# Optimization experiments

Hardware: AMD Instinct MI355X
Metric: run time of the kernel (lower is better)

## Reference

```python
import jax, jax.numpy as jnp
import numpy as np

D_MODEL = 1024
NUM_HEADS = 16
WINDOW = 2048  # must equal seq_len (see notes): source matmul attn(B,H,S,W) @ v(B,H,S,hd) requires W == S
SEQ_LEN = 2048
BATCH = 1


def setup_inputs() -> dict:
    key = jax.random.key(0)
    k0, k1, k2 = jax.random.split(key, 3)
    d = D_MODEL
    x = jax.random.normal(k0, (BATCH, SEQ_LEN, d), dtype=jnp.float32)
    w_qkv = jax.random.normal(k1, (3 * d, d), dtype=jnp.float32) * (d ** -0.5)
    b_qkv = jnp.zeros((3 * d,), dtype=jnp.float32)
    w_proj = jax.random.normal(k2, (d, d), dtype=jnp.float32) * (d ** -0.5)
    b_proj = jnp.zeros((d,), dtype=jnp.float32)
    return {"x": x, "w_qkv": w_qkv, "b_qkv": b_qkv, "w_proj": w_proj, "b_proj": b_proj}


def reference(x, w_qkv, b_qkv, w_proj, b_proj):
    B, S, d = x.shape
    H = NUM_HEADS
    hd = d // H
    W = WINDOW
    scale = hd ** -0.5

    # qkv projection (torch Linear: x @ W^T + b)
    qkv = x @ w_qkv.T + b_qkv                      # (B, S, 3d)
    qkv = qkv.reshape(B, S, 3, H, hd).transpose(2, 0, 3, 1, 4)  # (3, B, H, S, hd)
    q, k, v = qkv[0], qkv[1], qkv[2]

    # sliding-window scores: score[b,h,i,j] = q_i . k_padded[i+j] * scale, j in [0, W)
    pad = W // 2
    k_pad = jnp.pad(k, ((0, 0), (0, 0), (pad, pad), (0, 0)))     # (B, H, S+W, hd)
    scores_full = jnp.einsum('bhid,bhjd->bhij', q, k_pad) * scale  # (B, H, S, S+W)
    idx = jnp.arange(S)[:, None] + jnp.arange(W)[None, :]          # (S, W) banded gather indices
    scores = jnp.take_along_axis(scores_full, idx[None, None], axis=-1)  # (B, H, S, W)

    attn = jax.nn.softmax(scores, axis=-1)
    attn = jnp.nan_to_num(attn)  # faithful to torch.nan_to_num(attn, 0.0)

    # Faithful to the source: forward() does matmul(attn, v), i.e. column j of the
    # windowed attn indexes v position j directly (requires W == S).
    out = jnp.einsum('bhij,bhjd->bhid', attn, v)   # (B, H, S, hd)
    out = out.transpose(0, 2, 1, 3).reshape(B, S, d)
    out = out @ w_proj.T + b_proj
    return out, attn
```

## Files before the change

### kernel.cpp

```cpp
#include <hip/hip_runtime.h>
#include <hip/hip_bf16.h>

typedef __hip_bfloat16 bf16;
typedef __attribute__((ext_vector_type(8))) short short8;
typedef __attribute__((ext_vector_type(4))) float f32x4;
typedef __attribute__((ext_vector_type(4))) unsigned short ushort4v;

#define DEV static __device__ __forceinline__

static constexpr int SEQ = 2048;
static constexpr int DM  = 1024;
static constexpr int NH  = 16;
static constexpr int HD  = 64;
static constexpr int WIN = 2048;
static constexpr int PAD = 1024;

DEV void async16(const void* g, void* l) {
  __builtin_amdgcn_global_load_lds(
      (__attribute__((address_space(1))) void*)(g),
      (__attribute__((address_space(3))) void*)(l), 16, 0, 0);
}

__global__ __launch_bounds__(256) void k_cvt(const float* __restrict__ x,
                                             const float* __restrict__ wq,
                                             const float* __restrict__ wp,
                                             bf16* __restrict__ xb,
                                             bf16* __restrict__ wqb,
                                             bf16* __restrict__ wpb) {
  const int NX = SEQ * DM, NQ = 3 * DM * DM, NP = DM * DM;
  const int tot = (NX + NQ + NP) >> 2;
  const int stride = gridDim.x * 256;
  for (int i = blockIdx.x * 256 + threadIdx.x; i < tot; i += stride) {
    int e = i << 2;
    const float* s; bf16* d; int o;
    if (e < NX)            { s = x;  d = xb;  o = e; }
    else if (e < NX + NQ)  { s = wq; d = wqb; o = e - NX; }
    else                   { s = wp; d = wpb; o = e - NX - NQ; }
    float4 v = *(const float4*)(s + o);
    __align__(8) bf16 t4[4] = {__float2bfloat16(v.x), __float2bfloat16(v.y),
                               __float2bfloat16(v.z), __float2bfloat16(v.w)};
    *(uint2*)(d + o) = *(uint2*)t4;
  }
}

DEV void gemm_core64(const bf16* __restrict__ A, const bf16* __restrict__ B,
                     int m0, int n0, int K, int tid, bf16* As, bf16* Bs,
                     f32x4 (&acc)[4][2]) {
  const int lane = tid & 63, wid = tid >> 6;
  const int l15 = lane & 15, l4 = lane >> 4;
  for (int k0 = 0; k0 < K; k0 += 64) {
    __syncthreads();
    #pragma unroll
    for (int it = 0; it < 2; ++it) {
      int rb = it * 32 + wid * 8;
      int r  = rb + (lane >> 3);
      int c  = (lane & 7) * 8;
      async16(A + (size_t)(m0 + r) * K + k0 + c, As + rb * 64);
    }
    #pragma unroll
    for (int it = 0; it < 4; ++it) {
      int rb = it * 32 + wid * 8;
      int r  = rb + (lane >> 3);
      int c  = (lane & 7) * 8;
      async16(B + (size_t)(n0 + r) * K + k0 + c, Bs + rb * 64);
    }
    asm volatile("s_waitcnt vmcnt(0)" ::: "memory");
    __syncthreads();
    #pragma unroll
    for (int kk = 0; kk < 2; ++kk) {
      short8 a[4], b[2];
      #pragma unroll
      for (int im = 0; im < 4; ++im)
        a[im] = *(const short8*)(As + (im * 16 + l15) * 64 + kk * 32 + l4 * 8);
      #pragma unroll
      for (int in = 0; in < 2; ++in)
        b[in] = *(const short8*)(Bs + (wid * 32 + in * 16 + l15) * 64 + kk * 32 + l4 * 8);
      #pragma unroll
      for (int im = 0; im < 4; ++im)
        #pragma unroll
        for (int in = 0; in < 2; ++in)
          acc[im][in] = __builtin_amdgcn_mfma_f32_16x16x32_bf16(a[im], b[in], acc[im][in], 0, 0, 0);
    }
  }
}

__global__ __launch_bounds__(256) void k_gemm_qkv(const bf16* __restrict__ A,
                                                  const bf16* __restrict__ B,
                                                  const float* __restrict__ bias,
                                                  bf16* __restrict__ qo,
                                                  bf16* __restrict__ ko,
                                                  bf16* __restrict__ vt) {
  __shared__ bf16 As[64 * 64], Bs[128 * 64];
  const int tid = threadIdx.x, lane = tid & 63;
  const int wid = tid >> 6;
  const int l15 = lane & 15, l4 = lane >> 4;
  const int m0 = blockIdx.x * 64, n0 = blockIdx.y * 128;
  f32x4 acc[4][2] = {};
  gemm_core64(A, B, m0, n0, DM, tid, As, Bs, acc);
  #pragma unroll
  for (int im = 0; im < 4; ++im)
    #pragma unroll
    for (int in = 0; in < 2; ++in) {
      int col = n0 + wid * 32 + in * 16 + l15;
      float bval = bias[col];
      int t = col >> 10, h = (col >> 6) & 15, dd = col & 63;
      int row0 = m0 + im * 16 + l4 * 4;
      if (t == 2) {
        __align__(8) bf16 t4[4];
        #pragma unroll
        for (int r = 0; r < 4; ++r)
          t4[r] = __float2bfloat16(acc[im][in][r] + bval);
        *(uint2*)&vt[((size_t)h * HD + dd) * SEQ + row0] = *(uint2*)t4;
      } else {
        #pragma unroll
        for (int r = 0; r < 4; ++r) {
          float v = acc[im][in][r] + bval;
          size_t idx = ((size_t)h * SEQ + row0 + r) * HD + dd;
          if (t == 0) qo[idx] = __float2bfloat16(v * 0.18033688011112042f);
          else        ko[idx] = __float2bfloat16(v);
        }
      }
    }
}

DEV void stage_kp(const bf16* kbase, int i0, int tt, int lane, bf16* dst) {
  #pragma unroll
  for (int it = 0; it < 4; ++it) {
    int r  = it * 8 + (lane >> 3);
    int cg = lane & 7;
    int jp = i0 + tt * 32 + r;
    int krow = jp - PAD;
    krow = krow < 0 ? 0 : (krow > SEQ - 1 ? SEQ - 1 : krow);
    int sc = (cg ^ (r & 7)) * 8;
    async16(kbase + (size_t)krow * HD + sc, dst + it * 8 * 64);
  }
}

DEV void qk_mfma_lds(const bf16* KPb, const short8 (&qf)[2][2], int l15, int l4,
                     f32x4 (&sf)[2][2]) {
  __builtin_amdgcn_s_setprio(1);
  #pragma unroll
  for (int kg = 0; kg < 2; ++kg) {
    short8 kfr[2];
    #pragma unroll
    for (int fn = 0; fn < 2; ++fn) {
      int jl = fn * 16 + l15;
      int pg = (kg * 4 + l4) ^ (jl & 7);
      kfr[fn] = *(const short8*)&KPb[jl * 64 + pg * 8];
    }
    #pragma unroll
    for (int fm = 0; fm < 2; ++fm)
      #pragma unroll
      for (int fn = 0; fn < 2; ++fn)
        sf[fm][fn] = __builtin_amdgcn_mfma_f32_16x16x32_bf16(qf[fm][kg], kfr[fn], sf[fm][fn], 0, 0, 0);
  }
  __builtin_amdgcn_s_setprio(0);
}

DEV void qk_mfma_lds_sw(const bf16* KPb, const short8 (&qf)[2][2], int l15, int l4,
                        f32x4 (&sf)[2][2]) {
  __builtin_amdgcn_s_setprio(1);
  #pragma unroll
  for (int kg = 0; kg < 2; ++kg) {
    short8 kfr[2];
    #pragma unroll
    for (int fj = 0; fj < 2; ++fj) {
      int jl = fj * 16 + l15;
      int pg = (kg * 4 + l4) ^ (jl & 7);
      kfr[fj] = *(const short8*)&KPb[jl * 64 + pg * 8];
    }
    #pragma unroll
    for (int fj = 0; fj < 2; ++fj)
      #pragma unroll
      for (int fi = 0; fi < 2; ++fi)
        sf[fj][fi] = __builtin_amdgcn_mfma_f32_16x16x32_bf16(kfr[fj], qf[fi][kg], sf[fj][fi], 0, 0, 0);
  }
  __builtin_amdgcn_s_setprio(0);
}

DEV int pad_lo(int i0) { int d = PAD - i0; return d <= 0 ? 0 : (d >> 5); }
DEV int pad_hi(int i0) { int t = ((PAD + SEQ - 1 - i0) >> 5) + 1; return t > 65 ? 65 : t; }

__global__ __launch_bounds__(256) void k_attn(const bf16* __restrict__ q,
                                              const bf16* __restrict__ kkk,
                                              const bf16* __restrict__ vT,
                                              float* __restrict__ attn,
                                              bf16* __restrict__ ao) {
  const int wgid = (blockIdx.x & 7) * 128 + (blockIdx.x >> 3);
  const int h  = wgid >> 6;
  const int i0 = (wgid & 63) << 5;
  const int tid = threadIdx.x;
  const int c = tid >> 6;
  const int lane = tid & 63;
  const int l15 = lane & 15, l4 = lane >> 4;
  const int lo_g = pad_lo(i0), hi_g = pad_hi(i0);

  __shared__ bf16 KP[4][2][32 * 64];
  __shared__ unsigned short JFB[4][32 * 64];
  __shared__ float sums[4][32];
  __shared__ float invL[32];

  short8 qf[2][2];
  #pragma unroll
  for (int fm = 0; fm < 2; ++fm)
    #pragma unroll
    for (int kg = 0; kg < 2; ++kg)
      qf[fm][kg] = *(const short8*)&q[((size_t)h * SEQ + i0 + fm * 16 + l15) * HD + kg * 32 + l4 * 8];

  const bf16* kbase = kkk + (size_t)h * SEQ * HD;
  const bf16* vbase = vT + (size_t)h * HD * SEQ;
  float* abase = attn + (size_t)(h * SEQ + i0) * WIN;

  {
    constexpr int st[5] = {0, 16, 32, 48, 65};
    int lo = st[c] > lo_g ? st[c] : lo_g;
    int hi = st[c + 1] < hi_g ? st[c + 1] : hi_g;

    float psum[2] = {0.f, 0.f};
    if (lo < hi) {
      stage_kp(kbase, i0, lo, lane, KP[c][lo & 1]);
      for (int tt = lo; tt < hi; ++tt) {
        int nxt = (tt + 1 < hi) ? tt + 1 : tt;
        stage_kp(kbase, i0, nxt, lane, KP[c][(tt + 1) & 1]);
        asm volatile("s_waitcnt vmcnt(4)" ::: "memory");
        f32x4 sf[2][2] = {};
        qk_mfma_lds_sw(KP[c][tt & 1], qf, l15, l4, sf);
        const bool interior = (tt >= 1) && (tt <= 63) &&
                              (i0 + tt * 32 >= PAD) && (i0 + tt * 32 + 31 < PAD + SEQ);
        if (interior) {
          #pragma unroll
          for (int fj = 0; fj < 2; ++fj)
            #pragma unroll
            for (int r = 0; r < 4; ++r) {
              psum[0] += __builtin_amdgcn_exp2f(sf[fj][0][r]);
              psum[1] += __builtin_amdgcn_exp2f(sf[fj][1][r]);
            }
        } else {
          #pragma unroll
          for (int fj = 0; fj < 2; ++fj)
            #pragma unroll
            for (int r = 0; r < 4; ++r) {
              int jj = tt * 32 + fj * 16 + l4 * 4 + r;
              int jp = i0 + jj;
              bool pad = (jp < PAD) || (jp >= PAD + SEQ);
              #pragma unroll
              for (int fi = 0; fi < 2; ++fi) {
                int iloc = fi * 16 + l15;
                float e = pad ? 1.0f : __builtin_amdgcn_exp2f(sf[fj][fi][r]);
                if ((unsigned)(jj - iloc) < (unsigned)WIN) psum[fi] += e;
              }
            }
        }
      }
    }
    float r0 = psum[0];
    r0 += __shfl_xor(r0, 16); r0 += __shfl_xor(r0, 32);
    float r1 = psum[1];
    r1 += __shfl_xor(r1, 16); r1 += __shfl_xor(r1, 32);
    if (lane < 32) {
      int i_abs = i0 + lane;
      float s = (lane < 16) ? r0 : r1;
      if (c == 0) {
        int cl = i0 + lo_g * 32 - i_abs; if (cl < 0) cl = 0;
        int cr = i_abs + WIN - (i0 + hi_g * 32); if (cr < 0) cr = 0;
        s += (float)(cl + cr);
      }
      sums[c][lane] = s;
    }
  }
  __syncthreads();
  if (tid < 32)
    invL[tid] = __builtin_amdgcn_rcpf(sums[0][tid] + sums[1][tid] +
                                      sums[2][tid] + sums[3][tid]);
  __syncthreads();

  float invf[4];
  #pragma unroll
  for (int s2 = 0; s2 < 4; ++s2) invf[s2] = invL[s2 * 8 + (lane >> 3)];

  const int c0 = c * 16, c1 = c0 + 16;
  unsigned short* JW = JFB[c];
  f32x4 oacc[2][4] = {};
  stage_kp(kbase, i0, c0, lane, KP[c][0]);
  for (int tt = c0; tt <= c1; ++tt) {
    short8 bv[4];
    if (tt > c0) {
      int jb = (tt - 1) * 32;
      #pragma unroll
      for (int nd = 0; nd < 4; ++nd)
        bv[nd] = *(const short8*)&vbase[(size_t)(nd * 16 + l15) * SEQ + jb + l4 * 8];
    }
    int nxt = (tt < c1) ? tt + 1 : tt;
    stage_kp(kbase, i0, nxt, lane, KP[c][(tt + 1) & 1]);
    if (tt == c0)          asm volatile("s_waitcnt vmcnt(4)" ::: "memory");
    else if (tt == c0 + 1) asm volatile("s_waitcnt vmcnt(8)" ::: "memory");
    else                   asm volatile("s_waitcnt vmcnt(12)" ::: "memory");

    const bool fp = (tt < lo_g) || (tt >= hi_g);
    f32x4 sf[2][2] = {};
    if (!fp) qk_mfma_lds(KP[c][tt & 1], qf, l15, l4, sf);

    const bool allv = (i0 + tt * 32 >= PAD) && (i0 + tt * 32 + 31 < PAD + SEQ);
    #pragma unroll
    for (int fm = 0; fm < 2; ++fm)
      #pragma unroll
      for (int fn = 0; fn < 2; ++fn) {
        int J0 = tt * 32 + fn * 16 + l15;
        bool padc = fp || (!allv && ((i0 + J0 < PAD) || (i0 + J0 >= PAD + SEQ)));
        #pragma unroll
        for (int r = 0; r < 4; ++r) {
          int row = fm * 16 + l4 * 4 + r;
          float e = padc ? 1.0f : __builtin_amdgcn_exp2f(sf[fm][fn][r]);
          int j6 = (J0 - row) & 63;
          int sg = (j6 >> 3) ^ (row & 7);
          JW[row * 64 + sg * 8 + (j6 & 7)] = __bfloat16_as_ushort(__float2bfloat16(e));
        }
      }

    if (tt > c0) {
      const int g = (tt - 1) & 1;
      const int Jb = (tt - 1) * 32;
      const int c8 = lane & 7;
      #pragma unroll
      for (int s2 = 0; s2 < 4; ++s2) {
        int row = s2 * 8 + (lane >> 3);
        int sg = (g * 4 + (c8 >> 1)) ^ (row & 7);
        ushort4v uv = *(const ushort4v*)&JW[row * 64 + sg * 8 + (c8 & 1) * 4];
        f32x4 vv;
        #pragma unroll
        for (int e = 0; e < 4; ++e)
          vv[e] = __uint_as_float((unsigned)uv[e] << 16) * invf[s2];
        *(f32x4*)(abase + (size_t)row * WIN + Jb + c8 * 4) = vv;
      }
      short8 af[2];
      #pragma unroll
      for (int fm = 0; fm < 2; ++fm) {
        int row = fm * 16 + l15;
        int sg = (g * 4 + l4) ^ (row & 7);
        af[fm] = *(const short8*)&JW[row * 64 + sg * 8];
      }
      __builtin_amdgcn_s_setprio(1);
      #pragma unroll
      for (int fm = 0; fm < 2; ++fm)
        #pragma unroll
        for (int nd = 0; nd < 4; ++nd)
          oacc[fm][nd] = __builtin_amdgcn_mfma_f32_16x16x32_bf16(af[fm], bv[nd], oacc[fm][nd], 0, 0, 0);
      __builtin_amdgcn_s_setprio(0);
    }
  }

  __syncthreads();
  float* OX = (float*)&KP[0][0][0];
  float* OW = OX + c * 2048;
  #pragma unroll
  for (int fm = 0; fm < 2; ++fm)
    #pragma unroll
    for (int nd = 0; nd < 4; ++nd)
      #pragma unroll
      for (int r = 0; r < 4; ++r)
        OW[(fm * 16 + l4 * 4 + r) * 64 + nd * 16 + l15] = oacc[fm][nd][r];
  __syncthreads();
  {
    int row = tid >> 3;
    int d0 = (tid & 7) * 8;
    float iv = invL[row];
    union { unsigned short u[8]; short8 v; } o;
    #pragma unroll
    for (int e = 0; e < 8; ++e) {
      int idx = row * 64 + d0 + e;
      float s = (OX[idx] + OX[2048 + idx] + OX[4096 + idx] + OX[6144 + idx]) * iv;
      o.u[e] = __bfloat16_as_ushort(__float2bfloat16(s));
    }
    *(short8*)&ao[(size_t)(i0 + row) * DM + h * HD + d0] = o.v;
  }
}

__global__ __launch_bounds__(256) void k_gemm_proj(const bf16* __restrict__ A,
                                                   const bf16* __restrict__ B,
                                                   const float* __restrict__ bias,
                                                   float* __restrict__ out) {
  __shared__ bf16 As[64 * 64], Bs[128 * 64];
  const int tid = threadIdx.x, lane = tid & 63;
  const int wid = tid >> 6;
  const int l15 = lane & 15, l4 = lane >> 4;
  const int m0 = blockIdx.x * 64, n0 = blockIdx.y * 128;
  f32x4 acc[4][2] = {};
  gemm_core64(A, B, m0, n0, DM, tid, As, Bs, acc);
  #pragma unroll
  for (int im = 0; im < 4; ++im)
    #pragma unroll
    for (int in = 0; in < 2; ++in) {
      int col = n0 + wid * 32 + in * 16 + l15;
      float bval = bias[col];
      #pragma unroll
      for (int r = 0; r < 4; ++r) {
        int row = m0 + im * 16 + l4 * 4 + r;
        out[(size_t)row * DM + col] = acc[im][in][r] + bval;
      }
    }
}

extern "C" void kernel_launch(void* const* d_in, const int* in_sizes, int n_in,
                              void* d_out, int out_size, void* d_ws, size_t ws_size,
                              hipStream_t stream) {
  (void)in_sizes; (void)n_in; (void)out_size; (void)ws_size;
  const float* x  = (const float*)d_in[0];
  const float* wq = (const float*)d_in[1];
  const float* bq = (const float*)d_in[2];
  const float* wp = (const float*)d_in[3];
  const float* bp = (const float*)d_in[4];
  float* out  = (float*)d_out;
  float* attn = out + (size_t)SEQ * DM;

  char* ws = (char*)d_ws;
  bf16* xb    = (bf16*)(ws + (size_t) 0);
  bf16* wqb   = (bf16*)(ws + ((size_t)4  << 20));
  bf16* wpb   = (bf16*)(ws + ((size_t)10 << 20));
  bf16* qarr  = (bf16*)(ws + ((size_t)12 << 20));
  bf16* karr  = (bf16*)(ws + ((size_t)16 << 20));
  bf16* vt    = (bf16*)(ws + ((size_t)24 << 20));
  bf16* ao    = (bf16*)(ws + ((size_t)28 << 20));

  k_cvt<<<dim3(1024), dim3(256), 0, stream>>>(x, wq, wp, xb, wqb, wpb);
  k_gemm_qkv<<<dim3(32, 24), dim3(256), 0, stream>>>(xb, wqb, bq, qarr, karr, vt);
  k_attn<<<dim3(1024), dim3(256), 0, stream>>>(qarr, karr, vt, attn, ao);
  k_gemm_proj<<<dim3(32, 8), dim3(256), 0, stream>>>(ao, wpb, bp, out);
}
```

Measured before the change: 145.8 us.

## Shrink attention LDS footprint by register-prefetching K and sharing one buffer

Merges the double-buffered K tiles and the probability buffer into a single shared array, halving LDS per block. In the second pass, the next K tile is prefetched into registers and written to LDS after the PV step, replacing the async global-to-LDS double buffer. It also requests four blocks per CU through launch bounds. The goal is higher occupancy to hide latency, at the cost of more registers and losing asynchronous LDS loads.

New measurement: 313.4 us. +115.0%, slower.

```diff
diff --git a/kernel.cpp b/kernel.cpp
--- a/kernel.cpp
+++ b/kernel.cpp
@@ -181,11 +181,11 @@
 DEV int pad_lo(int i0) { int d = PAD - i0; return d <= 0 ? 0 : (d >> 5); }
 DEV int pad_hi(int i0) { int t = ((PAD + SEQ - 1 - i0) >> 5) + 1; return t > 65 ? 65 : t; }
 
-__global__ __launch_bounds__(256) void k_attn(const bf16* __restrict__ q,
-                                              const bf16* __restrict__ kkk,
-                                              const bf16* __restrict__ vT,
-                                              float* __restrict__ attn,
-                                              bf16* __restrict__ ao) {
+__global__ __launch_bounds__(256, 4) void k_attn(const bf16* __restrict__ q,
+                                                 const bf16* __restrict__ kkk,
+                                                 const bf16* __restrict__ vT,
+                                                 float* __restrict__ attn,
+                                                 bf16* __restrict__ ao) {
   const int wgid = (blockIdx.x & 7) * 128 + (blockIdx.x >> 3);
   const int h  = wgid >> 6;
   const int i0 = (wgid & 63) << 5;
@@ -195,8 +195,7 @@
   const int l15 = lane & 15, l4 = lane >> 4;
   const int lo_g = pad_lo(i0), hi_g = pad_hi(i0);
 
-  __shared__ bf16 KP[4][2][32 * 64];
-  __shared__ unsigned short JFB[4][32 * 64];
+  __shared__ __align__(16) bf16 UB[4 * 4096];
   __shared__ float sums[4][32];
   __shared__ float invL[32];
 
@@ -212,19 +211,21 @@
   float* abase = attn + (size_t)(h * SEQ + i0) * WIN;
 
   {
+    bf16* B0 = UB + c * 4096;
+    bf16* B1 = UB + c * 4096 + 2048;
     constexpr int st[5] = {0, 16, 32, 48, 65};
     int lo = st[c] > lo_g ? st[c] : lo_g;
     int hi = st[c + 1] < hi_g ? st[c + 1] : hi_g;
 
     float psum[2] = {0.f, 0.f};
     if (lo < hi) {
-      stage_kp(kbase, i0, lo, lane, KP[c][lo & 1]);
+      stage_kp(kbase, i0, lo, lane, (lo & 1) ? B1 : B0);
       for (int tt = lo; tt < hi; ++tt) {
         int nxt = (tt + 1 < hi) ? tt + 1 : tt;
-        stage_kp(kbase, i0, nxt, lane, KP[c][(tt + 1) & 1]);
+        stage_kp(kbase, i0, nxt, lane, ((tt + 1) & 1) ? B1 : B0);
         asm volatile("s_waitcnt vmcnt(4)" ::: "memory");
         f32x4 sf[2][2] = {};
-        qk_mfma_lds_sw(KP[c][tt & 1], qf, l15, l4, sf);
+        qk_mfma_lds_sw((tt & 1) ? B1 : B0, qf, l15, l4, sf);
         const bool interior = (tt >= 1) && (tt <= 63) &&
                               (i0 + tt * 32 >= PAD) && (i0 + tt * 32 + 31 < PAD + SEQ);
         if (interior) {
@@ -279,10 +280,37 @@
   for (int s2 = 0; s2 < 4; ++s2) invf[s2] = invL[s2 * 8 + (lane >> 3)];
 
   const int c0 = c * 16, c1 = c0 + 16;
-  unsigned short* JW = JFB[c];
+  bf16* KPc = UB + c * 4096;
+  unsigned short* JW = (unsigned short*)(UB + c * 4096 + 2048);
+
+  {
+    short8 kr[4];
+    #pragma unroll
+    for (int it = 0; it < 4; ++it) {
+      int r = it * 8 + (lane >> 3), cg = lane & 7;
+      int jp = i0 + c0 * 32 + r;
+      int krow = jp - PAD;
+      krow = krow < 0 ? 0 : (krow > SEQ - 1 ? SEQ - 1 : krow);
+      kr[it] = *(const short8*)&kbase[(size_t)krow * HD + (cg ^ (r & 7)) * 8];
+    }
+    #pragma unroll
+    for (int it = 0; it < 4; ++it)
+      *(short8*)&KPc[it * 512 + lane * 8] = kr[it];
+  }
+
   f32x4 oacc[2][4] = {};
-  stage_kp(kbase, i0, c0, lane, KP[c][0]);
   for (int tt = c0; tt <= c1; ++tt) {
+    short8 krn[4];
+    if (tt < c1) {
+      #pragma unroll
+      for (int it = 0; it < 4; ++it) {
+        int r = it * 8 + (lane >> 3), cg = lane & 7;
+        int jp = i0 + (tt + 1) * 32 + r;
+        int krow = jp - PAD;
+        krow = krow < 0 ? 0 : (krow > SEQ - 1 ? SEQ - 1 : krow);
+        krn[it] = *(const short8*)&kbase[(size_t)krow * HD + (cg ^ (r & 7)) * 8];
+      }
+    }
     short8 bv[4];
     if (tt > c0) {
       int jb = (tt - 1) * 32;
@@ -290,15 +318,10 @@
       for (int nd = 0; nd < 4; ++nd)
         bv[nd] = *(const short8*)&vbase[(size_t)(nd * 16 + l15) * SEQ + jb + l4 * 8];
     }
-    int nxt = (tt < c1) ? tt + 1 : tt;
-    stage_kp(kbase, i0, nxt, lane, KP[c][(tt + 1) & 1]);
-    if (tt == c0)          asm volatile("s_waitcnt vmcnt(4)" ::: "memory");
-    else if (tt == c0 + 1) asm volatile("s_waitcnt vmcnt(8)" ::: "memory");
-    else                   asm volatile("s_waitcnt vmcnt(12)" ::: "memory");
 
     const bool fp = (tt < lo_g) || (tt >= hi_g);
     f32x4 sf[2][2] = {};
-    if (!fp) qk_mfma_lds(KP[c][tt & 1], qf, l15, l4, sf);
+    if (!fp) qk_mfma_lds(KPc, qf, l15, l4, sf);
 
     const bool allv = (i0 + tt * 32 >= PAD) && (i0 + tt * 32 + 31 < PAD + SEQ);
     #pragma unroll
@@ -347,10 +370,16 @@
           oacc[fm][nd] = __builtin_amdgcn_mfma_f32_16x16x32_bf16(af[fm], bv[nd], oacc[fm][nd], 0, 0, 0);
       __builtin_amdgcn_s_setprio(0);
     }
+
+    if (tt < c1) {
+      #pragma unroll
+      for (int it = 0; it < 4; ++it)
+        *(short8*)&KPc[it * 512 + lane * 8] = krn[it];
+    }
   }
 
   __syncthreads();
-  float* OX = (float*)&KP[0][0][0];
+  float* OX = (float*)UB;
   float* OW = OX + c * 2048;
   #pragma unroll
   for (int fm = 0; fm < 2; ++fm)
```

## Process two 32-row tiles per attention block with two-way column split

Applied to the files above, without the earlier changes.

Each attention workgroup now covers 64 query rows, as two 32-row tiles, instead of 32 rows. The four waves are paired: each pair shares one row tile and splits the key columns in halves rather than quarters. The grid is halved to 512 blocks, and the reduction of the per-wave row sums and output partials is reorganised to match. The aim is to cut per-wave setup and cross-wave reduction overhead by giving each wave longer loops, at the cost of fewer workgroups to fill the GPU and a longer serial chain per wave.

New measurement: 155.2 us. 6.5% more time.

```diff
diff --git a/kernel.cpp b/kernel.cpp
--- a/kernel.cpp
+++ b/kernel.cpp
@@ -186,19 +186,22 @@
                                               const bf16* __restrict__ vT,
                                               float* __restrict__ attn,
                                               bf16* __restrict__ ao) {
-  const int wgid = (blockIdx.x & 7) * 128 + (blockIdx.x >> 3);
-  const int h  = wgid >> 6;
-  const int i0 = (wgid & 63) << 5;
+  const int nbid = (blockIdx.x & 7) * 64 + (blockIdx.x >> 3);
+  const int h  = nbid >> 5;
+  const int ib = nbid & 31;
   const int tid = threadIdx.x;
-  const int c = tid >> 6;
+  const int c  = tid >> 6;
+  const int ri = c >> 1;
+  const int cc = c & 1;
   const int lane = tid & 63;
   const int l15 = lane & 15, l4 = lane >> 4;
+  const int i0 = ib * 64 + ri * 32;
   const int lo_g = pad_lo(i0), hi_g = pad_hi(i0);
 
   __shared__ bf16 KP[4][2][32 * 64];
   __shared__ unsigned short JFB[4][32 * 64];
   __shared__ float sums[4][32];
-  __shared__ float invL[32];
+  __shared__ float invL[2][32];
 
   short8 qf[2][2];
   #pragma unroll
@@ -212,9 +215,9 @@
   float* abase = attn + (size_t)(h * SEQ + i0) * WIN;
 
   {
-    constexpr int st[5] = {0, 16, 32, 48, 65};
-    int lo = st[c] > lo_g ? st[c] : lo_g;
-    int hi = st[c + 1] < hi_g ? st[c + 1] : hi_g;
+    constexpr int st[3] = {0, 32, 65};
+    int lo = st[cc] > lo_g ? st[cc] : lo_g;
+    int hi = st[cc + 1] < hi_g ? st[cc + 1] : hi_g;
 
     float psum[2] = {0.f, 0.f};
     if (lo < hi) {
@@ -260,7 +263,7 @@
     if (lane < 32) {
       int i_abs = i0 + lane;
       float s = (lane < 16) ? r0 : r1;
-      if (c == 0) {
+      if (cc == 0) {
         int cl = i0 + lo_g * 32 - i_abs; if (cl < 0) cl = 0;
         int cr = i_abs + WIN - (i0 + hi_g * 32); if (cr < 0) cr = 0;
         s += (float)(cl + cr);
@@ -269,16 +272,17 @@
     }
   }
   __syncthreads();
-  if (tid < 32)
-    invL[tid] = __builtin_amdgcn_rcpf(sums[0][tid] + sums[1][tid] +
-                                      sums[2][tid] + sums[3][tid]);
+  if (tid < 64) {
+    int rt = tid >> 5, row = tid & 31;
+    invL[rt][row] = __builtin_amdgcn_rcpf(sums[rt * 2][row] + sums[rt * 2 + 1][row]);
+  }
   __syncthreads();
 
   float invf[4];
   #pragma unroll
-  for (int s2 = 0; s2 < 4; ++s2) invf[s2] = invL[s2 * 8 + (lane >> 3)];
-
-  const int c0 = c * 16, c1 = c0 + 16;
+  for (int s2 = 0; s2 < 4; ++s2) invf[s2] = invL[ri][s2 * 8 + (lane >> 3)];
+
+  const int c0 = cc * 32, c1 = c0 + 32;
   unsigned short* JW = JFB[c];
   f32x4 oacc[2][4] = {};
   stage_kp(kbase, i0, c0, lane, KP[c][0]);
@@ -361,17 +365,19 @@
         OW[(fm * 16 + l4 * 4 + r) * 64 + nd * 16 + l15] = oacc[fm][nd][r];
   __syncthreads();
   {
-    int row = tid >> 3;
-    int d0 = (tid & 7) * 8;
-    float iv = invL[row];
-    union { unsigned short u[8]; short8 v; } o;
-    #pragma unroll
-    for (int e = 0; e < 8; ++e) {
-      int idx = row * 64 + d0 + e;
-      float s = (OX[idx] + OX[2048 + idx] + OX[4096 + idx] + OX[6144 + idx]) * iv;
-      o.u[e] = __bfloat16_as_ushort(__float2bfloat16(s));
-    }
-    *(short8*)&ao[(size_t)(i0 + row) * DM + h * HD + d0] = o.v;
+    int row64 = tid >> 2;
+    int rt = row64 >> 5, r32 = row64 & 31;
+    int d0 = (tid & 3) * 16;
+    const float* pA = OX + (rt * 2) * 2048 + r32 * 64;
+    const float* pB = OX + (rt * 2 + 1) * 2048 + r32 * 64;
+    float iv = invL[rt][r32];
+    union { unsigned short u[16]; short8 v[2]; } o;
+    #pragma unroll
+    for (int e = 0; e < 16; ++e)
+      o.u[e] = __bfloat16_as_ushort(__float2bfloat16((pA[d0 + e] + pB[d0 + e]) * iv));
+    bf16* op = &ao[(size_t)(ib * 64 + row64) * DM + h * HD + d0];
+    *(short8*)op = o.v[0];
+    *(short8*)(op + 8) = o.v[1];
   }
 }
 
@@ -423,6 +429,6 @@
 
   k_cvt<<<dim3(1024), dim3(256), 0, stream>>>(x, wq, wp, xb, wqb, wpb);
   k_gemm_qkv<<<dim3(32, 24), dim3(256), 0, stream>>>(xb, wqb, bq, qarr, karr, vt);
-  k_attn<<<dim3(1024), dim3(256), 0, stream>>>(qarr, karr, vt, attn, ao);
+  k_attn<<<dim3(512), dim3(256), 0, stream>>>(qarr, karr, vt, attn, ao);
   k_gemm_proj<<<dim3(32, 8), dim3(256), 0, stream>>>(ao, wpb, bp, out);
 }
```
